# Optimization experiments

Measured on AMD Instinct MI355X. Metric: run time of the kernel, lower is better.

The kernel has to match this reference:

```python
import jax, jax.numpy as jnp
import numpy as np

N_NODES = 100_000
N_RAND_EDGES = 3_200_000
IN_FEATS, HIDDEN, N_CLASSES = 256, 32, 40


def setup_inputs() -> dict:
    key = jax.random.key(0)
    kf, ks, kd, kw1, kw2 = jax.random.split(key, 5)
    features = jax.random.normal(kf, (N_NODES, IN_FEATS), dtype=jnp.float32)
    # random edges + explicit self loops (mirrors dgl.add_self_loop)
    src = jnp.concatenate([
        jax.random.randint(ks, (N_RAND_EDGES,), 0, N_NODES, dtype=jnp.int32),
        jnp.arange(N_NODES, dtype=jnp.int32),
    ])
    dst = jnp.concatenate([
        jax.random.randint(kd, (N_RAND_EDGES,), 0, N_NODES, dtype=jnp.int32),
        jnp.arange(N_NODES, dtype=jnp.int32),
    ])
    # Glorot-style init as in DGL GraphConv
    W1 = jax.random.normal(kw1, (IN_FEATS, HIDDEN), dtype=jnp.float32) * (2.0 / (IN_FEATS + HIDDEN)) ** 0.5
    b1 = jnp.zeros((HIDDEN,), dtype=jnp.float32)
    W2 = jax.random.normal(kw2, (HIDDEN, N_CLASSES), dtype=jnp.float32) * (2.0 / (HIDDEN + N_CLASSES)) ** 0.5
    b2 = jnp.zeros((N_CLASSES,), dtype=jnp.float32)
    return {"features": features, "src": src, "dst": dst,
            "W1": W1, "b1": b1, "W2": W2, "b2": b2}


def _graph_conv(x, W, b, src, dst, norm_src, norm_dst):
    """DGL GraphConv, norm='both': D_in^{-1/2} A D_out^{-1/2} X W + b.
    Apply W first (cheaper gather when out_feats small); math-identical."""
    h = (x * norm_src[:, None]) @ W              # [N, out]
    msgs = h[src]                                # gather  [E, out]
    agg = jax.ops.segment_sum(msgs, dst, num_segments=N_NODES)  # scatter-add
    return agg * norm_dst[:, None] + b


def reference(features, src, dst, W1, b1, W2, b2):
    ones = jnp.ones(src.shape[0], dtype=jnp.float32)
    out_deg = jax.ops.segment_sum(ones, src, num_segments=N_NODES)
    in_deg = jax.ops.segment_sum(ones, dst, num_segments=N_NODES)
    norm_src = jax.lax.rsqrt(out_deg)            # self loops guarantee deg >= 1
    norm_dst = jax.lax.rsqrt(in_deg)

    x = _graph_conv(features, W1, b1, src, dst, norm_src, norm_dst)
    x = jax.nn.relu(x)
    # F.dropout(training=self.training) is identity at inference
    x = _graph_conv(x, W2, b2, src, dst, norm_src, norm_dst)
    return jax.nn.log_softmax(x, axis=1)
```

## Files before the change

### kernel.cpp

```cpp
#include <hip/hip_runtime.h>
#include <hip/hip_bf16.h>
#include <math.h>

#define BSHIFT 7
#define NBUCK(N) (((N) + 127) >> 7)
#define TILE 8192
#define CAP 5632

typedef short bf16x8 __attribute__((ext_vector_type(8)));
typedef float f32x16 __attribute__((ext_vector_type(16)));

__device__ __forceinline__ unsigned short f2bf(float f) {
    unsigned u = __float_as_uint(f);
    u += 0x7fffu + ((u >> 16) & 1u);
    return (unsigned short)(u >> 16);
}
__device__ __forceinline__ unsigned packbf2(float lo, float hi) {
    return (unsigned)f2bf(lo) | ((unsigned)f2bf(hi) << 16);
}
__device__ __forceinline__ float bf_lo(unsigned u) { return __uint_as_float(u << 16); }
__device__ __forceinline__ float bf_hi(unsigned u) { return __uint_as_float(u & 0xffff0000u); }

__global__ __launch_bounds__(256) void pg_kernel(
    const int* __restrict__ src, const int* __restrict__ dst,
    int* __restrict__ gcurD, int* __restrict__ gcurS,
    int* __restrict__ gbufD, unsigned char* __restrict__ gbufS,
    const float* __restrict__ feat, const float* __restrict__ W1,
    unsigned short* __restrict__ h1, int E, int K, int PB, int N) {
    __shared__ char smem[16896];
    const int t = threadIdx.x;

    if (blockIdx.x < PB) {
        int* cD = (int*)smem;
        int* bD = cD + 800;
        int* cS = bD + 800;
        int* bS = cS + 800;
        const int tile = blockIdx.x * TILE;
        for (int i = t; i < K; i += 256) { cD[i] = 0; cS[i] = 0; }
        __syncthreads();

        int dv[32];
        #pragma unroll
        for (int i = 0; i < 32; ++i) {
            const int e = tile + i * 256 + t;
            dv[i] = (e < E) ? dst[e] : -1;
            if (dv[i] >= 0) {
                atomicAdd(&cD[dv[i] >> BSHIFT], 1);
                atomicAdd(&cS[src[e] >> BSHIFT], 1);
            }
        }
        __syncthreads();
        for (int i = t; i < K; i += 256) {
            int c = cD[i];
            bD[i] = (c ? atomicAdd(&gcurD[i], c) : 0) + i * CAP;
            cD[i] = 0;
            c = cS[i];
            bS[i] = (c ? atomicAdd(&gcurS[i], c) : 0) + i * CAP;
            cS[i] = 0;
        }
        __syncthreads();
        #pragma unroll
        for (int i = 0; i < 32; ++i) {
            if (dv[i] >= 0) {
                const int e = tile + i * 256 + t;
                const int sv = src[e];
                const int b1 = dv[i] >> BSHIFT;
                const int p1 = bD[b1] + atomicAdd(&cD[b1], 1);
                gbufD[p1] = ((dv[i] & 127) << 17) | sv;
                const int b2 = sv >> BSHIFT;
                const int p2 = bS[b2] + atomicAdd(&cS[b2], 1);
                gbufS[p2] = (unsigned char)(sv & 127);
            }
        }
    } else {
        short* W1t = (short*)smem;
        for (int i = t; i < 8192; i += 256) {
            const int k = i >> 5, c = i & 31;
            W1t[c * 264 + k] = (short)f2bf(W1[i]);
        }
        __syncthreads();

        const int l  = t & 63;
        const int wv = t >> 6;
        const int base = (blockIdx.x - PB) * 128 + wv * 32;
        const int m  = l & 31;
        const int kh = (l >> 5) << 3;
        int r = base + m;
        if (r >= N) r = N - 1;
        const float* fr = feat + (size_t)r * 256 + kh;
        const short* wr = &W1t[m * 264 + kh];

        f32x16 acc;
        #pragma unroll
        for (int i = 0; i < 16; ++i) acc[i] = 0.f;

        #pragma unroll
        for (int kb = 0; kb < 16; ++kb) {
            const float4 f0 = *(const float4*)(fr + kb * 16);
            const float4 f1 = *(const float4*)(fr + kb * 16 + 4);
            bf16x8 a;
            a[0] = (short)f2bf(f0.x); a[1] = (short)f2bf(f0.y);
            a[2] = (short)f2bf(f0.z); a[3] = (short)f2bf(f0.w);
            a[4] = (short)f2bf(f1.x); a[5] = (short)f2bf(f1.y);
            a[6] = (short)f2bf(f1.z); a[7] = (short)f2bf(f1.w);
            const bf16x8 b = *(const bf16x8*)(wr + kb * 16);
            acc = __builtin_amdgcn_mfma_f32_32x32x16_bf16(a, b, acc, 0, 0, 0);
        }

        const int rbase = base + ((l >> 5) << 2);
        #pragma unroll
        for (int reg = 0; reg < 16; ++reg) {
            const int row = rbase + (reg & 3) + ((reg >> 2) << 3);
            if (row < N)
                h1[(size_t)row * 32 + m] = f2bf(acc[reg]);
        }
    }
}

__global__ __launch_bounds__(256) void fillS_kernel(
    const int* __restrict__ cntS, const unsigned char* __restrict__ gbufS,
    float* __restrict__ nsrc, int N, int K) {
    __shared__ int cnt[128];
    const int t = threadIdx.x;
    const int b = blockIdx.x;
    if (t < 128) cnt[t] = 0;
    __syncthreads();
    const int bs = b * CAP;
    const int be = bs + min(cntS[b], CAP);
    for (int idx = bs + t; idx < be; idx += 256)
        atomicAdd(&cnt[gbufS[idx]], 1);
    __syncthreads();
    const int n = (b << BSHIFT) + t;
    if (t < 128 && n < N) nsrc[n] = rsqrtf((float)cnt[t]);
}

__global__ __launch_bounds__(512) void fda1_kernel(
    const int* __restrict__ cntD, int* __restrict__ gbufD,
    const unsigned* __restrict__ h1, const float* __restrict__ nsrc,
    const float* __restrict__ b1, int* __restrict__ rowstart,
    int* __restrict__ indeg, float* __restrict__ ndst,
    unsigned* __restrict__ x1s, int N, int K) {
    __shared__ int lraw[CAP];
    __shared__ int lcsr[CAP];
    __shared__ int cnt[128], sc[128], cur[128];
    __shared__ float sb1[32];
    const int t = threadIdx.x;
    const int b = blockIdx.x;
    if (t < 128) cnt[t] = 0;
    if (t >= 128 && t < 160) sb1[t - 128] = b1[t - 128];
    __syncthreads();

    const int bs = b * CAP;
    const int total = min(cntD[b], CAP);
    for (int i = t; i < total; i += 512) {
        const int v = gbufD[bs + i];
        lraw[i] = v;
        atomicAdd(&cnt[v >> 17], 1);
    }
    __syncthreads();
    if (t < 128) sc[t] = cnt[t];
    __syncthreads();
    for (int off = 1; off < 128; off <<= 1) {
        int x = (t < 128 && t >= off) ? sc[t - off] : 0;
        __syncthreads();
        if (t < 128) sc[t] += x;
        __syncthreads();
    }
    if (t < 128) {
        const int deg = cnt[t];
        cur[t] = sc[t] - deg;
        const int n = (b << BSHIFT) + t;
        if (n < N) {
            rowstart[n] = bs + sc[t] - deg;
            indeg[n] = deg;
            ndst[n] = rsqrtf((float)deg);
        }
    }
    __syncthreads();
    for (int i = t; i < total; i += 512) {
        const int v = lraw[i];
        const int pos = atomicAdd(&cur[v >> 17], 1);
        lcsr[pos] = v & 131071;
    }
    __syncthreads();
    for (int i = t; i < total; i += 512) gbufD[bs + i] = lcsr[i];

    const int node = t >> 2;
    const int c = t & 3;
    const int n = (b << BSHIFT) + node;
    if (n >= N) return;
    const int deg = cnt[node];
    const int re = sc[node];
    int k = re - deg;
    float a0=0.f,a1=0.f,a2=0.f,a3=0.f,a4=0.f,a5=0.f,a6=0.f,a7=0.f;
    float d0=0.f,d1=0.f,d2=0.f,d3=0.f,d4=0.f,d5=0.f,d6=0.f,d7=0.f;
    const uint4* H = (const uint4*)h1;
    for (; k + 3 < re; k += 4) {
        const int s0 = lcsr[k],     s1 = lcsr[k + 1];
        const int s2 = lcsr[k + 2], s3 = lcsr[k + 3];
        const uint4 q0 = H[(size_t)s0 * 4 + c];
        const uint4 q1 = H[(size_t)s1 * 4 + c];
        const uint4 q2 = H[(size_t)s2 * 4 + c];
        const uint4 q3 = H[(size_t)s3 * 4 + c];
        const float w0 = nsrc[s0], w1 = nsrc[s1];
        const float w2 = nsrc[s2], w3 = nsrc[s3];
        a0 += bf_lo(q0.x)*w0; a1 += bf_hi(q0.x)*w0;
        a2 += bf_lo(q0.y)*w0; a3 += bf_hi(q0.y)*w0;
        a4 += bf_lo(q0.z)*w0; a5 += bf_hi(q0.z)*w0;
        a6 += bf_lo(q0.w)*w0; a7 += bf_hi(q0.w)*w0;
        d0 += bf_lo(q1.x)*w1; d1 += bf_hi(q1.x)*w1;
        d2 += bf_lo(q1.y)*w1; d3 += bf_hi(q1.y)*w1;
        d4 += bf_lo(q1.z)*w1; d5 += bf_hi(q1.z)*w1;
        d6 += bf_lo(q1.w)*w1; d7 += bf_hi(q1.w)*w1;
        a0 += bf_lo(q2.x)*w2; a1 += bf_hi(q2.x)*w2;
        a2 += bf_lo(q2.y)*w2; a3 += bf_hi(q2.y)*w2;
        a4 += bf_lo(q2.z)*w2; a5 += bf_hi(q2.z)*w2;
        a6 += bf_lo(q2.w)*w2; a7 += bf_hi(q2.w)*w2;
        d0 += bf_lo(q3.x)*w3; d1 += bf_hi(q3.x)*w3;
        d2 += bf_lo(q3.y)*w3; d3 += bf_hi(q3.y)*w3;
        d4 += bf_lo(q3.z)*w3; d5 += bf_hi(q3.z)*w3;
        d6 += bf_lo(q3.w)*w3; d7 += bf_hi(q3.w)*w3;
    }
    for (; k < re; ++k) {
        const int s0 = lcsr[k];
        const uint4 q0 = H[(size_t)s0 * 4 + c];
        const float w0 = nsrc[s0];
        a0 += bf_lo(q0.x)*w0; a1 += bf_hi(q0.x)*w0;
        a2 += bf_lo(q0.y)*w0; a3 += bf_hi(q0.y)*w0;
        a4 += bf_lo(q0.z)*w0; a5 += bf_hi(q0.z)*w0;
        a6 += bf_lo(q0.w)*w0; a7 += bf_hi(q0.w)*w0;
    }
    a0 += d0; a1 += d1; a2 += d2; a3 += d3;
    a4 += d4; a5 += d5; a6 += d6; a7 += d7;
    const float nd = rsqrtf((float)deg);
    const float ns = nsrc[n];
    const float* bb = sb1 + c * 8;
    float x0 = fmaxf(a0 * nd + bb[0], 0.f) * ns;
    float x1 = fmaxf(a1 * nd + bb[1], 0.f) * ns;
    float x2 = fmaxf(a2 * nd + bb[2], 0.f) * ns;
    float x3 = fmaxf(a3 * nd + bb[3], 0.f) * ns;
    float x4 = fmaxf(a4 * nd + bb[4], 0.f) * ns;
    float x5 = fmaxf(a5 * nd + bb[5], 0.f) * ns;
    float x6 = fmaxf(a6 * nd + bb[6], 0.f) * ns;
    float x7 = fmaxf(a7 * nd + bb[7], 0.f) * ns;
    uint4 o;
    o.x = packbf2(x0, x1); o.y = packbf2(x2, x3);
    o.z = packbf2(x4, x5); o.w = packbf2(x6, x7);
    ((uint4*)x1s)[(size_t)n * 4 + c] = o;
}

__global__ __launch_bounds__(256) void agg2f_kernel(
    const int* __restrict__ csr_src, const int* __restrict__ rowstart,
    const int* __restrict__ indeg, const unsigned* __restrict__ x1s,
    const float* __restrict__ ndst, const float* __restrict__ W2,
    const float* __restrict__ b2, float* __restrict__ out, int N) {
    __shared__ float sW2[32 * 40];
    __shared__ float sb2[40];
    const int t = threadIdx.x;
    for (int i = t; i < 1280; i += 256) sW2[i] = W2[i];
    if (t < 40) sb2[t] = b2[t];
    __syncthreads();
    const int n = blockIdx.x * 64 + (t >> 2);
    if (n >= N) return;
    const int c = t & 3;
    const int rs = rowstart[n];
    const int re = rs + indeg[n];
    float a0=0.f,a1=0.f,a2=0.f,a3=0.f,a4=0.f,a5=0.f,a6=0.f,a7=0.f;
    float d0=0.f,d1=0.f,d2=0.f,d3=0.f,d4=0.f,d5=0.f,d6=0.f,d7=0.f;
    const uint4* H = (const uint4*)x1s;
    int k = rs;
    for (; k + 3 < re; k += 4) {
        const int s0 = csr_src[k],     s1 = csr_src[k + 1];
        const int s2 = csr_src[k + 2], s3 = csr_src[k + 3];
        const uint4 q0 = H[(size_t)s0 * 4 + c];
        const uint4 q1 = H[(size_t)s1 * 4 + c];
        const uint4 q2 = H[(size_t)s2 * 4 + c];
        const uint4 q3 = H[(size_t)s3 * 4 + c];
        a0 += bf_lo(q0.x); a1 += bf_hi(q0.x);
        a2 += bf_lo(q0.y); a3 += bf_hi(q0.y);
        a4 += bf_lo(q0.z); a5 += bf_hi(q0.z);
        a6 += bf_lo(q0.w); a7 += bf_hi(q0.w);
        d0 += bf_lo(q1.x); d1 += bf_hi(q1.x);
        d2 += bf_lo(q1.y); d3 += bf_hi(q1.y);
        d4 += bf_lo(q1.z); d5 += bf_hi(q1.z);
        d6 += bf_lo(q1.w); d7 += bf_hi(q1.w);
        a0 += bf_lo(q2.x); a1 += bf_hi(q2.x);
        a2 += bf_lo(q2.y); a3 += bf_hi(q2.y);
        a4 += bf_lo(q2.z); a5 += bf_hi(q2.z);
        a6 += bf_lo(q2.w); a7 += bf_hi(q2.w);
        d0 += bf_lo(q3.x); d1 += bf_hi(q3.x);
        d2 += bf_lo(q3.y); d3 += bf_hi(q3.y);
        d4 += bf_lo(q3.z); d5 += bf_hi(q3.z);
        d6 += bf_lo(q3.w); d7 += bf_hi(q3.w);
    }
    for (; k < re; ++k) {
        const int s0 = csr_src[k];
        const uint4 q0 = H[(size_t)s0 * 4 + c];
        a0 += bf_lo(q0.x); a1 += bf_hi(q0.x);
        a2 += bf_lo(q0.y); a3 += bf_hi(q0.y);
        a4 += bf_lo(q0.z); a5 += bf_hi(q0.z);
        a6 += bf_lo(q0.w); a7 += bf_hi(q0.w);
    }
    a0 += d0; a1 += d1; a2 += d2; a3 += d3;
    a4 += d4; a5 += d5; a6 += d6; a7 += d7;
    const float nd = ndst[n];
    const float v0 = a0 * nd, v1 = a1 * nd, v2 = a2 * nd, v3 = a3 * nd;
    const float v4 = a4 * nd, v5 = a5 * nd, v6 = a6 * nd, v7 = a7 * nd;

    float z[10];
    #pragma unroll
    for (int u = 0; u < 10; ++u) z[u] = sb2[c * 10 + u];
    const int gbase = (t & 63) & ~3;
    #pragma unroll
    for (int cc = 0; cc < 4; ++cc) {
        const int sl = gbase | cc;
        const float w0 = __shfl(v0, sl, 64);
        const float w1 = __shfl(v1, sl, 64);
        const float w2 = __shfl(v2, sl, 64);
        const float w3 = __shfl(v3, sl, 64);
        const float w4 = __shfl(v4, sl, 64);
        const float w5 = __shfl(v5, sl, 64);
        const float w6 = __shfl(v6, sl, 64);
        const float w7 = __shfl(v7, sl, 64);
        const float* Wr = &sW2[(cc * 8) * 40 + c * 10];
        #pragma unroll
        for (int u = 0; u < 10; ++u) {
            z[u] += w0 * Wr[u]       + w1 * Wr[40 + u]  + w2 * Wr[80 + u]  + w3 * Wr[120 + u]
                  + w4 * Wr[160 + u] + w5 * Wr[200 + u] + w6 * Wr[240 + u] + w7 * Wr[280 + u];
        }
    }
    float m = z[0];
    #pragma unroll
    for (int u = 1; u < 10; ++u) m = fmaxf(m, z[u]);
    m = fmaxf(m, __shfl_xor(m, 1, 64));
    m = fmaxf(m, __shfl_xor(m, 2, 64));
    float s = 0.f;
    #pragma unroll
    for (int u = 0; u < 10; ++u) s += __expf(z[u] - m);
    s += __shfl_xor(s, 1, 64);
    s += __shfl_xor(s, 2, 64);
    const float ls = __logf(s);
    float* op = out + (size_t)n * 40 + c * 10;
    #pragma unroll
    for (int u = 0; u < 10; ++u) op[u] = z[u] - m - ls;
}

extern "C" void kernel_launch(void* const* d_in, const int* in_sizes, int n_in,
                              void* d_out, int out_size, void* d_ws, size_t ws_size,
                              hipStream_t stream) {
    const float* feat = (const float*)d_in[0];
    const int*   src  = (const int*)d_in[1];
    const int*   dst  = (const int*)d_in[2];
    const float* W1   = (const float*)d_in[3];
    const float* b1   = (const float*)d_in[4];
    const float* W2   = (const float*)d_in[5];
    const float* b2   = (const float*)d_in[6];
    float* out = (float*)d_out;

    const int N = in_sizes[0] / 256;
    const int E = in_sizes[1];
    const int K = NBUCK(N);

    char* p = (char*)d_ws;
    float* nsrc = (float*)p;                 p += (size_t)N * 4;
    float* ndst = (float*)p;                 p += (size_t)N * 4;
    unsigned* h1  = (unsigned*)p;            p += (size_t)N * 64;
    unsigned* x1s = (unsigned*)p;            p += (size_t)N * 64;
    char* a2dead = (char*)p;                 p += (size_t)N * 128;
    int* rowstart = (int*)p;                 p += (size_t)N * 4;
    int* indeg_i  = (int*)p;                 p += (size_t)N * 4;
    int* gcurD    = (int*)p;                 p += 800 * 4;
    int* gcurS    = (int*)p;                 p += 800 * 4;
    int* gbufD    = (int*)p;                 p += (size_t)K * CAP * 4;
    unsigned char* gbufS = (unsigned char*)a2dead;

    hipMemsetAsync(gcurD, 0, sizeof(int) * 1600, stream);

    const int PB = (E + TILE - 1) / TILE;
    const int GB = (N + 127) / 128;

    pg_kernel<<<PB + GB, 256, 0, stream>>>(src, dst, gcurD, gcurS, gbufD, gbufS,
                                           feat, W1, (unsigned short*)h1, E, K, PB, N);
    fillS_kernel<<<K, 256, 0, stream>>>(gcurS, gbufS, nsrc, N, K);
    fda1_kernel<<<K, 512, 0, stream>>>(gcurD, gbufD, h1, nsrc, b1,
                                       rowstart, indeg_i, ndst, x1s, N, K);
    agg2f_kernel<<<(N + 63) / 64, 256, 0, stream>>>(gbufD, rowstart, indeg_i, x1s, ndst, W2, b2, out, N);
}
```

Measured before the change: 384.5 us.

## Replace source-degree bucketing with global atomic out-degree counts

```diff
diff --git a/kernel.cpp b/kernel.cpp
--- a/kernel.cpp
+++ b/kernel.cpp
@@ -23,8 +23,8 @@
 
 __global__ __launch_bounds__(256) void pg_kernel(
     const int* __restrict__ src, const int* __restrict__ dst,
-    int* __restrict__ gcurD, int* __restrict__ gcurS,
-    int* __restrict__ gbufD, unsigned char* __restrict__ gbufS,
+    int* __restrict__ gcurD, int* __restrict__ outdeg,
+    int* __restrict__ gbufD,
     const float* __restrict__ feat, const float* __restrict__ W1,
     unsigned short* __restrict__ h1, int E, int K, int PB, int N) {
     __shared__ char smem[16896];
@@ -33,10 +33,8 @@
     if (blockIdx.x < PB) {
         int* cD = (int*)smem;
         int* bD = cD + 800;
-        int* cS = bD + 800;
-        int* bS = cS + 800;
         const int tile = blockIdx.x * TILE;
-        for (int i = t; i < K; i += 256) { cD[i] = 0; cS[i] = 0; }
+        for (int i = t; i < K; i += 256) cD[i] = 0;
         __syncthreads();
 
         int dv[32];
@@ -46,17 +44,14 @@
             dv[i] = (e < E) ? dst[e] : -1;
             if (dv[i] >= 0) {
                 atomicAdd(&cD[dv[i] >> BSHIFT], 1);
-                atomicAdd(&cS[src[e] >> BSHIFT], 1);
+                atomicAdd(&outdeg[src[e]], 1);
             }
         }
         __syncthreads();
         for (int i = t; i < K; i += 256) {
-            int c = cD[i];
+            const int c = cD[i];
             bD[i] = (c ? atomicAdd(&gcurD[i], c) : 0) + i * CAP;
             cD[i] = 0;
-            c = cS[i];
-            bS[i] = (c ? atomicAdd(&gcurS[i], c) : 0) + i * CAP;
-            cS[i] = 0;
         }
         __syncthreads();
         #pragma unroll
@@ -67,9 +62,6 @@
                 const int b1 = dv[i] >> BSHIFT;
                 const int p1 = bD[b1] + atomicAdd(&cD[b1], 1);
                 gbufD[p1] = ((dv[i] & 127) << 17) | sv;
-                const int b2 = sv >> BSHIFT;
-                const int p2 = bS[b2] + atomicAdd(&cS[b2], 1);
-                gbufS[p2] = (unsigned char)(sv & 127);
             }
         }
     } else {
@@ -117,26 +109,9 @@
     }
 }
 
-__global__ __launch_bounds__(256) void fillS_kernel(
-    const int* __restrict__ cntS, const unsigned char* __restrict__ gbufS,
-    float* __restrict__ nsrc, int N, int K) {
-    __shared__ int cnt[128];
-    const int t = threadIdx.x;
-    const int b = blockIdx.x;
-    if (t < 128) cnt[t] = 0;
-    __syncthreads();
-    const int bs = b * CAP;
-    const int be = bs + min(cntS[b], CAP);
-    for (int idx = bs + t; idx < be; idx += 256)
-        atomicAdd(&cnt[gbufS[idx]], 1);
-    __syncthreads();
-    const int n = (b << BSHIFT) + t;
-    if (t < 128 && n < N) nsrc[n] = rsqrtf((float)cnt[t]);
-}
-
 __global__ __launch_bounds__(512) void fda1_kernel(
     const int* __restrict__ cntD, int* __restrict__ gbufD,
-    const unsigned* __restrict__ h1, const float* __restrict__ nsrc,
+    const unsigned* __restrict__ h1, const int* __restrict__ outdeg,
     const float* __restrict__ b1, int* __restrict__ rowstart,
     int* __restrict__ indeg, float* __restrict__ ndst,
     unsigned* __restrict__ x1s, int N, int K) {
@@ -202,8 +177,10 @@
         const uint4 q1 = H[(size_t)s1 * 4 + c];
         const uint4 q2 = H[(size_t)s2 * 4 + c];
         const uint4 q3 = H[(size_t)s3 * 4 + c];
-        const float w0 = nsrc[s0], w1 = nsrc[s1];
-        const float w2 = nsrc[s2], w3 = nsrc[s3];
+        const float w0 = rsqrtf((float)outdeg[s0]);
+        const float w1 = rsqrtf((float)outdeg[s1]);
+        const float w2 = rsqrtf((float)outdeg[s2]);
+        const float w3 = rsqrtf((float)outdeg[s3]);
         a0 += bf_lo(q0.x)*w0; a1 += bf_hi(q0.x)*w0;
         a2 += bf_lo(q0.y)*w0; a3 += bf_hi(q0.y)*w0;
         a4 += bf_lo(q0.z)*w0; a5 += bf_hi(q0.z)*w0;
@@ -224,7 +201,7 @@
     for (; k < re; ++k) {
         const int s0 = lcsr[k];
         const uint4 q0 = H[(size_t)s0 * 4 + c];
-        const float w0 = nsrc[s0];
+        const float w0 = rsqrtf((float)outdeg[s0]);
         a0 += bf_lo(q0.x)*w0; a1 += bf_hi(q0.x)*w0;
         a2 += bf_lo(q0.y)*w0; a3 += bf_hi(q0.y)*w0;
         a4 += bf_lo(q0.z)*w0; a5 += bf_hi(q0.z)*w0;
@@ -233,7 +210,7 @@
     a0 += d0; a1 += d1; a2 += d2; a3 += d3;
     a4 += d4; a5 += d5; a6 += d6; a7 += d7;
     const float nd = rsqrtf((float)deg);
-    const float ns = nsrc[n];
+    const float ns = rsqrtf((float)outdeg[n]);
     const float* bb = sb1 + c * 8;
     float x0 = fmaxf(a0 * nd + bb[0], 0.f) * ns;
     float x1 = fmaxf(a1 * nd + bb[1], 0.f) * ns;
@@ -362,27 +339,23 @@
     const int K = NBUCK(N);
 
     char* p = (char*)d_ws;
-    float* nsrc = (float*)p;                 p += (size_t)N * 4;
-    float* ndst = (float*)p;                 p += (size_t)N * 4;
+    int* outdeg   = (int*)p;                 p += (size_t)N * 4;
+    int* gcurD    = (int*)p;                 p += 800 * 4;
+    float* ndst   = (float*)p;               p += (size_t)N * 4;
     unsigned* h1  = (unsigned*)p;            p += (size_t)N * 64;
     unsigned* x1s = (unsigned*)p;            p += (size_t)N * 64;
-    char* a2dead = (char*)p;                 p += (size_t)N * 128;
     int* rowstart = (int*)p;                 p += (size_t)N * 4;
     int* indeg_i  = (int*)p;                 p += (size_t)N * 4;
-    int* gcurD    = (int*)p;                 p += 800 * 4;
-    int* gcurS    = (int*)p;                 p += 800 * 4;
     int* gbufD    = (int*)p;                 p += (size_t)K * CAP * 4;
-    unsigned char* gbufS = (unsigned char*)a2dead;
-
-    hipMemsetAsync(gcurD, 0, sizeof(int) * 1600, stream);
+
+    hipMemsetAsync(outdeg, 0, (size_t)N * 4 + 800 * 4, stream);
 
     const int PB = (E + TILE - 1) / TILE;
     const int GB = (N + 127) / 128;
 
-    pg_kernel<<<PB + GB, 256, 0, stream>>>(src, dst, gcurD, gcurS, gbufD, gbufS,
+    pg_kernel<<<PB + GB, 256, 0, stream>>>(src, dst, gcurD, outdeg, gbufD,
                                            feat, W1, (unsigned short*)h1, E, K, PB, N);
-    fillS_kernel<<<K, 256, 0, stream>>>(gcurS, gbufS, nsrc, N, K);
-    fda1_kernel<<<K, 512, 0, stream>>>(gcurD, gbufD, h1, nsrc, b1,
+    fda1_kernel<<<K, 512, 0, stream>>>(gcurD, gbufD, h1, outdeg, b1,
                                        rowstart, indeg_i, ndst, x1s, N, K);
     agg2f_kernel<<<(N + 63) / 64, 256, 0, stream>>>(gbufD, rowstart, indeg_i, x1s, ndst, W2, b2, out, N);
 }
```

New measurement: 412.5 us. +7.3%, slower.
